# Kernel optimization log

Measured on AMD Instinct MI355X. Metric: run time of the kernel, lower is better.

Reference implementation:

```python
import jax, jax.numpy as jnp
import numpy as np
from jax import lax

T = 16          # timesteps
EPS = 1e-12     # torch F.normalize eps
DN = ('NCHW', 'OIHW', 'NCHW')

def conv2d(x, w, pad):
    return lax.conv_general_dilated(x, w, (1, 1), [(pad, pad), (pad, pad)],
                                    dimension_numbers=DN)

def setup_inputs() -> dict:
    key = jax.random.key(0)
    ks = jax.random.split(key, 7)
    B, C, H, W, K = 16, 512, 14, 14, 64
    return {
        'input_tensor': jax.random.normal(ks[0], (B * T, C, H, W), jnp.float32),
        'centers': jax.random.normal(ks[1], (K, C), jnp.float32) * 0.05,
        'share_w': jax.random.normal(ks[2], (K, C, 1, 1), jnp.float32) * 0.05,
        'share_b': jax.random.uniform(ks[3], (K,), jnp.float32),
        'U_z': jax.random.normal(ks[4], (K, K, 3, 3), jnp.float32) * 0.05,
        'U_r': jax.random.normal(ks[5], (K, K, 3, 3), jnp.float32) * 0.05,
        'U_h': jax.random.normal(ks[6], (K, K, 3, 3), jnp.float32) * 0.05,
    }

def reference(input_tensor, centers, share_w, share_b, U_z, U_r, U_h):
    NT, C, H, W = input_tensor.shape
    B = NT // T
    K = centers.shape[0]

    # soft-assignment pre-activation: 1x1 conv (SAME) -> [B*T, K, H, W]
    wxb = conv2d(input_tensor, share_w, 0) + share_b[None, :, None, None]
    wxb = wxb.reshape(B, T, K, H, W).transpose(1, 0, 2, 3, 4)  # [T,B,K,H,W]

    def gru_step(h, wxb_t):
        z = jax.nn.sigmoid(wxb_t + conv2d(h, U_z, 1))
        r = jax.nn.sigmoid(wxb_t + conv2d(h, U_r, 1))
        hh = jnp.tanh(wxb_t + conv2d(r * h, U_h, 1))
        h_new = (1.0 - z) * hh + z * h
        return h_new, h_new

    h0 = jnp.zeros((B, K, H, W), input_tensor.dtype)
    _, assign = lax.scan(gru_step, h0, wxb)            # [T,B,K,H,W]
    assign = assign.transpose(1, 0, 2, 3, 4).reshape(B * T, K, H * W)

    a_sum = assign.sum(-1, keepdims=True)              # [BT,K,1]
    a = a_sum * centers[None]                          # [BT,K,C]
    feats = input_tensor.reshape(B * T, C, H * W)
    x = jnp.einsum('nks,ncs->nkc', assign, feats)      # [BT,K,C]

    vlad = (x - a).reshape(B, T, K, C).sum(1)          # [B,K,C]
    vlad = vlad / jnp.maximum(jnp.linalg.norm(vlad, axis=2, keepdims=True), EPS)
    vlad = vlad.reshape(B, K * C)
    vlad = vlad / jnp.maximum(jnp.linalg.norm(vlad, axis=1, keepdims=True), EPS)
    return vlad
```

## Files before the change

kernel.cpp:

```cpp
#include <hip/hip_runtime.h>

#define Bc 16
#define Tc 16
#define Cc 512
#define Kc 64
#define Sc 196
#define KS (Kc*Sc)
#define BKS (Bc*Kc*Sc)
#define TBKS (Tc*BKS)
#define GFIN (16*64*512)
#define PART_N (8*GFIN)
#define PX 256
#define PLB2 (Kc*PX)

typedef __attribute__((ext_vector_type(8))) short bf16x8;
typedef __attribute__((ext_vector_type(4))) float f32x4;

__device__ __forceinline__ float sigmoid_f(float x) { return 1.f / (1.f + __expf(-x)); }
__device__ __forceinline__ float tanh_f(float x) { return 1.f - 2.f / (__expf(2.f * x) + 1.f); }

__device__ __forceinline__ float b2f(unsigned short u) {
    return __uint_as_float(((unsigned)u) << 16);
}
__device__ __forceinline__ unsigned short f2b(float f) {
    unsigned u = __float_as_uint(f);
    return (unsigned short)((u + 0x7FFFu + ((u >> 16) & 1u)) >> 16);
}
__device__ __forceinline__ void split1(float f, unsigned short& h, unsigned short& l) {
    unsigned u = __float_as_uint(f);
    unsigned uh = u & 0xffff0000u;
    h = (unsigned short)(uh >> 16);
    float fl = f - __uint_as_float(uh);
    l = (unsigned short)(__float_as_uint(fl) >> 16);
}

__device__ __forceinline__ float dpp_prev(float v) {
    return __int_as_float(__builtin_amdgcn_mov_dpp(__float_as_int(v), 0x111, 0xf, 0xf, true));
}
__device__ __forceinline__ float dpp_next(float v) {
    return __int_as_float(__builtin_amdgcn_mov_dpp(__float_as_int(v), 0x101, 0xf, 0xf, true));
}

__global__ __launch_bounds__(256) void k_prep_w(const float* __restrict__ w,
        unsigned short* __restrict__ wh, unsigned short* __restrict__ wl) {
    int idx = blockIdx.x * 256 + threadIdx.x;
    unsigned short h, l;
    split1(w[idx], h, l);
    wh[idx] = h; wl[idx] = l;
}

__global__ __launch_bounds__(256) void k_init(float4* __restrict__ h32,
        float4* __restrict__ h16, float4* __restrict__ rh16) {
    const int i = blockIdx.x * 256 + threadIdx.x;
    const float4 z = make_float4(0.f, 0.f, 0.f, 0.f);
    h32[i] = z;
    if (i < 32768) { h16[i] = z; rh16[i] = z; }
}

__global__ __launch_bounds__(512) void k_conv1x1(const float* __restrict__ x,
        const unsigned short* __restrict__ wh, const unsigned short* __restrict__ wl,
        const float* __restrict__ bias, float* __restrict__ wxb,
        float* __restrict__ assign0, float* __restrict__ hplane32,
        unsigned short* __restrict__ hplane16) {
    __shared__ unsigned short Xh[64 * 40];
    __shared__ unsigned short Xl[64 * 40];
    const int gs0 = blockIdx.x * 64;
    const int tid = threadIdx.x;
    const int wv = tid >> 6, lane = tid & 63;
    const int lg = lane >> 4, ln = lane & 15;
    const int mt = wv & 3, np = wv >> 2;
    const int gslS = tid & 63;
    const int c4S = (tid >> 6) * 4;
    const int gsS = gs0 + gslS;
    const int nS = gsS / Sc, sS = gsS - nS * Sc;
    const float* xcol = x + (size_t)nS * (Cc * Sc) + sS;
    const int colS = (((c4S >> 3) ^ ((gslS >> 3) & 3)) << 3) + (c4S & 7);
    const int kA = np * 32 + ln;
    const float bias0 = bias[kA], bias1 = bias[kA + 16];
    const int gsA = mt * 16 + ln;
    const int swzA = (gsA >> 3) & 3;

    float xr[4];
#pragma unroll
    for (int i = 0; i < 4; ++i) xr[i] = xcol[(size_t)(c4S + i) * Sc];

    f32x4 acc0 = {0.f, 0.f, 0.f, 0.f}, acc1 = {0.f, 0.f, 0.f, 0.f};
    for (int c0 = 0; c0 < Cc; c0 += 32) {
        __syncthreads();
        {
            ushort4 h, l;
            split1(xr[0], h.x, l.x); split1(xr[1], h.y, l.y);
            split1(xr[2], h.z, l.z); split1(xr[3], h.w, l.w);
            *(ushort4*)(Xh + gslS * 40 + colS) = h;
            *(ushort4*)(Xl + gslS * 40 + colS) = l;
        }
        __syncthreads();
        if (c0 + 32 < Cc) {
#pragma unroll
            for (int i = 0; i < 4; ++i) xr[i] = xcol[(size_t)(c0 + 32 + c4S + i) * Sc];
        }
        bf16x8 B0h = *(const bf16x8*)(wh + (size_t)kA * Cc + c0 + lg * 8);
        bf16x8 B0l = *(const bf16x8*)(wl + (size_t)kA * Cc + c0 + lg * 8);
        bf16x8 B1h = *(const bf16x8*)(wh + (size_t)(kA + 16) * Cc + c0 + lg * 8);
        bf16x8 B1l = *(const bf16x8*)(wl + (size_t)(kA + 16) * Cc + c0 + lg * 8);
        bf16x8 Af = *(const bf16x8*)(Xh + gsA * 40 + ((lg ^ swzA) << 3));
        bf16x8 Alo = *(const bf16x8*)(Xl + gsA * 40 + ((lg ^ swzA) << 3));
        acc0 = __builtin_amdgcn_mfma_f32_16x16x32_bf16(Af, B0h, acc0, 0, 0, 0);
        acc0 = __builtin_amdgcn_mfma_f32_16x16x32_bf16(Alo, B0h, acc0, 0, 0, 0);
        acc0 = __builtin_amdgcn_mfma_f32_16x16x32_bf16(Af, B0l, acc0, 0, 0, 0);
        acc1 = __builtin_amdgcn_mfma_f32_16x16x32_bf16(Af, B1h, acc1, 0, 0, 0);
        acc1 = __builtin_amdgcn_mfma_f32_16x16x32_bf16(Alo, B1h, acc1, 0, 0, 0);
        acc1 = __builtin_amdgcn_mfma_f32_16x16x32_bf16(Af, B1l, acc1, 0, 0, 0);
    }
#pragma unroll
    for (int r = 0; r < 4; ++r) {
        const int gs = gs0 + mt * 16 + lg * 4 + r;
        const int n = gs / Sc, s = gs - (gs / Sc) * Sc;
        const int t = n & 15, bb = n >> 4;
        const float v0 = acc0[r] + bias0;
        const float v1 = acc1[r] + bias1;
        const size_t rowbase = ((size_t)t * Bc + bb) * Kc;
        wxb[(rowbase + kA) * Sc + s] = v0;
        wxb[(rowbase + kA + 16) * Sc + s] = v1;
        if (t == 0) {
            const int px = (s / 14 + 1) * 16 + (s - (s / 14) * 14 + 1);
            const float a0 = (1.f - sigmoid_f(v0)) * tanh_f(v0);
            const float a1 = (1.f - sigmoid_f(v1)) * tanh_f(v1);
            assign0[((size_t)bb * Kc + kA) * Sc + s] = a0;
            assign0[((size_t)bb * Kc + kA + 16) * Sc + s] = a1;
            const size_t pp0 = (size_t)bb * PLB2 + (size_t)kA * PX + px;
            const size_t pp1 = (size_t)bb * PLB2 + (size_t)(kA + 16) * PX + px;
            hplane32[pp0] = a0; hplane16[pp0] = f2b(a0);
            hplane32[pp1] = a1; hplane16[pp1] = f2b(a1);
        }
    }
}

__global__ __launch_bounds__(512) void k_gru_gates(const unsigned short* __restrict__ hplane16,
        const float* __restrict__ wxb_t, const float* __restrict__ Uz, const float* __restrict__ Ur,
        float* __restrict__ zb, unsigned short* __restrict__ rhplane16) {
    extern __shared__ float lds[];
    unsigned short* P = (unsigned short*)lds;
    float* red = lds + 8192;
    const int b = blockIdx.x;
    const int k0 = blockIdx.y * 4;
    const int tid = threadIdx.x;
    const int wv = __builtin_amdgcn_readfirstlane(tid >> 6);
    const int lane = tid & 63;
    const int kp = wv >> 2, kiq = wv & 3;

    float preE[4]; bool valE[4]; size_t csE[4]; int kEa[4];
#pragma unroll
    for (int q = 0; q < 4; ++q) {
        const int o = tid + q * 512;
        const int set = o >> 8, px = o & 255;
        const int kp_o = set >> 2, r = set & 1;
        kEa[q] = k0 + kp_o * 2 + r;
        const int row = px >> 4, col = px & 15;
        valE[q] = (row >= 1 && row <= 14 && col >= 1 && col <= 14);
        csE[q] = ((size_t)b * Kc + kEa[q]) * Sc + (valE[q] ? (row - 1) * 14 + (col - 1) : 0);
        preE[q] = valE[q] ? wxb_t[csE[q]] : 0.f;
    }
    {
        const float4* src = (const float4*)(hplane16 + (size_t)b * PLB2);
        float4* dst = (float4*)P;
#pragma unroll
        for (int it = 0; it < 4; ++it) dst[it * 512 + tid] = src[it * 512 + tid];
    }
    __syncthreads();

    const int yp = lane >> 2, xq = (lane & 3) << 2;
    const int rowbase = (yp > 0) ? (yp - 1) : 0;
    const float* uz0 = Uz + (size_t)(k0 + kp * 2) * 576 + kiq * 144;
    const float* ur0 = Ur + (size_t)(k0 + kp * 2) * 576 + kiq * 144;
    float az[2][4] = {}, ar[2][4] = {};
    const unsigned short* Pw = P + (size_t)(kiq * 16) * PX + rowbase * 16 + xq;
#pragma unroll 2
    for (int ki = 0; ki < 16; ++ki) {
        const unsigned short* pk = Pw + ki * PX;
#pragma unroll
        for (int dy = 0; dy < 3; ++dy) {
            ushort4 u = *(const ushort4*)(pk + dy * 16);
            float4 m = make_float4(b2f(u.x), b2f(u.y), b2f(u.z), b2f(u.w));
            float e0 = dpp_prev(m.w);
            float e4 = dpp_next(m.x);
#pragma unroll
            for (int r = 0; r < 2; ++r) {
                const float* wz = uz0 + r * 576 + ki * 9 + dy * 3;
                float c0 = wz[0], c1 = wz[1], c2 = wz[2];
                az[r][0] += c0*e0  + c1*m.x + c2*m.y;
                az[r][1] += c0*m.x + c1*m.y + c2*m.z;
                az[r][2] += c0*m.y + c1*m.z + c2*m.w;
                az[r][3] += c0*m.z + c1*m.w + c2*e4;
                const float* wr = ur0 + r * 576 + ki * 9 + dy * 3;
                float d0 = wr[0], d1 = wr[1], d2 = wr[2];
                ar[r][0] += d0*e0  + d1*m.x + d2*m.y;
                ar[r][1] += d0*m.x + d1*m.y + d2*m.z;
                ar[r][2] += d0*m.y + d1*m.z + d2*m.w;
                ar[r][3] += d0*m.z + d1*m.w + d2*e4;
            }
        }
    }
    {
        float* rp = red + (size_t)wv * 1024 + lane;
#pragma unroll
        for (int r = 0; r < 2; ++r)
#pragma unroll
            for (int jj = 0; jj < 4; ++jj) {
                rp[(size_t)(r * 4 + jj) * 64] = az[r][jj];
                rp[(size_t)(8 + r * 4 + jj) * 64] = ar[r][jj];
            }
    }
    __syncthreads();
#pragma unroll
    for (int q = 0; q < 4; ++q) {
        const int o = tid + q * 512;
        const int set = o >> 8, px = o & 255;
        const int kp_o = set >> 2, g = (set >> 1) & 1, r = set & 1;
        const int lane_r = ((px >> 4) << 2) + ((px & 15) >> 2);
        const int v = (g * 2 + r) * 4 + (px & 3);
        float s0 = 0.f;
#pragma unroll
        for (int kq2 = 0; kq2 < 4; ++kq2)
            s0 += red[(size_t)((kp_o * 4 + kq2) * 16 + v) * 64 + lane_r];
        if (valE[q]) {
            float sv = sigmoid_f(preE[q] + s0);
            if (g == 0) {
                zb[csE[q]] = sv;
            } else {
                float hv = b2f(P[(size_t)kEa[q] * PX + px]);
                rhplane16[(size_t)b * PLB2 + (size_t)kEa[q] * PX + px] = f2b(sv * hv);
            }
        }
    }
}

__global__ __launch_bounds__(512) void k_gru_out(const unsigned short* __restrict__ rhplane16,
        const float* __restrict__ wxb_t, const float* __restrict__ Uh, const float* __restrict__ zb,
        float* __restrict__ hplane32, unsigned short* __restrict__ hplane16,
        float* __restrict__ assign_t) {
    extern __shared__ float lds[];
    unsigned short* P = (unsigned short*)lds;
    float* red = lds + 8192;
    const int b = blockIdx.x;
    const int k0 = blockIdx.y * 4;
    const int tid = threadIdx.x;
    const int wv = __builtin_amdgcn_readfirstlane(tid >> 6);
    const int lane = tid & 63;
    const int kp = wv >> 2, kiq = wv & 3;

    float preE[2], zvE[2], hpE[2]; bool valE[2]; size_t csE[2], ppE[2];
#pragma unroll
    for (int q = 0; q < 2; ++q) {
        const int o = tid + q * 512;
        const int set = o >> 8, px = o & 255;
        const int kp_o = set >> 1, r = set & 1;
        const int k = k0 + kp_o * 2 + r;
        const int row = px >> 4, col = px & 15;
        valE[q] = (row >= 1 && row <= 14 && col >= 1 && col <= 14);
        csE[q] = ((size_t)b * Kc + k) * Sc + (valE[q] ? (row - 1) * 14 + (col - 1) : 0);
        ppE[q] = (size_t)b * PLB2 + (size_t)k * PX + px;
        preE[q] = 0.f; zvE[q] = 0.f; hpE[q] = 0.f;
        if (valE[q]) {
            preE[q] = wxb_t[csE[q]];
            zvE[q] = zb[csE[q]];
            hpE[q] = hplane32[ppE[q]];
        }
    }
    {
        const float4* src = (const float4*)(rhplane16 + (size_t)b * PLB2);
        float4* dst = (float4*)P;
#pragma unroll
        for (int it = 0; it < 4; ++it) dst[it * 512 + tid] = src[it * 512 + tid];
    }
    __syncthreads();

    const int yp = lane >> 2, xq = (lane & 3) << 2;
    const int rowbase = (yp > 0) ? (yp - 1) : 0;
    const float* uh0 = Uh + (size_t)(k0 + kp * 2) * 576 + kiq * 144;
    float ah[2][4] = {};
    const unsigned short* Pw = P + (size_t)(kiq * 16) * PX + rowbase * 16 + xq;
#pragma unroll 2
    for (int ki = 0; ki < 16; ++ki) {
        const unsigned short* pk = Pw + ki * PX;
#pragma unroll
        for (int dy = 0; dy < 3; ++dy) {
            ushort4 u = *(const ushort4*)(pk + dy * 16);
            float4 m = make_float4(b2f(u.x), b2f(u.y), b2f(u.z), b2f(u.w));
            float e0 = dpp_prev(m.w);
            float e4 = dpp_next(m.x);
#pragma unroll
            for (int r = 0; r < 2; ++r) {
                const float* wh = uh0 + r * 576 + ki * 9 + dy * 3;
                float c0 = wh[0], c1 = wh[1], c2 = wh[2];
                ah[r][0] += c0*e0  + c1*m.x + c2*m.y;
                ah[r][1] += c0*m.x + c1*m.y + c2*m.z;
                ah[r][2] += c0*m.y + c1*m.z + c2*m.w;
                ah[r][3] += c0*m.z + c1*m.w + c2*e4;
            }
        }
    }
    {
        float* rp = red + (size_t)wv * 512 + lane;
#pragma unroll
        for (int r = 0; r < 2; ++r)
#pragma unroll
            for (int jj = 0; jj < 4; ++jj)
                rp[(size_t)(r * 4 + jj) * 64] = ah[r][jj];
    }
    __syncthreads();
#pragma unroll
    for (int q = 0; q < 2; ++q) {
        const int o = tid + q * 512;
        const int set = o >> 8, px = o & 255;
        const int kp_o = set >> 1, r = set & 1;
        const int lane_r = ((px >> 4) << 2) + ((px & 15) >> 2);
        const int v = r * 4 + (px & 3);
        float s0 = 0.f;
#pragma unroll
        for (int kq2 = 0; kq2 < 4; ++kq2)
            s0 += red[(size_t)((kp_o * 4 + kq2) * 8 + v) * 64 + lane_r];
        if (valE[q]) {
            float hh = tanh_f(preE[q] + s0);
            float hn = (1.f - zvE[q]) * hh + zvE[q] * hpE[q];
            hplane32[ppE[q]] = hn;
            hplane16[ppE[q]] = f2b(hn);
            assign_t[csE[q]] = hn;
        }
    }
}

__global__ __launch_bounds__(512) void k_einsum(const float* __restrict__ x, const float* __restrict__ assign,
                                                float* __restrict__ part) {
    extern __shared__ float lds[];
    unsigned short* Ah = (unsigned short*)lds;
    unsigned short* Al = Ah + 64 * 40;
    unsigned short* Xh = Al + 64 * 40;
    unsigned short* Xl = Xh + 128 * 40;
    const int cq = blockIdx.x, tg = blockIdx.y, b = blockIdx.z;
    const int tid = threadIdx.x;
    const int wv = tid >> 6, lane = tid & 63;
    const int lg = lane >> 4, ln = lane & 15;
    const int ka = tid >> 3, ss4 = (tid & 7) * 4;
    const int cx = tid >> 2, ss8 = (tid & 3) * 8;

    f32x4 acc[4];
#pragma unroll
    for (int mt = 0; mt < 4; ++mt) acc[mt] = (f32x4){0.f, 0.f, 0.f, 0.f};

    for (int tt = 0; tt < 2; ++tt) {
        const int t = tg * 2 + tt;
        const int n = b * Tc + t;
        const float* ap = assign + ((size_t)t * Bc + b) * KS;
        const float* xp = x + ((size_t)n * Cc + cq * 128) * Sc;
        for (int sc7 = 0; sc7 < 7; ++sc7) {
            const int s0 = sc7 * 32;
            __syncthreads();
            {
                float4 v = make_float4(0.f, 0.f, 0.f, 0.f);
                if (s0 + ss4 <= 192) v = *(const float4*)(ap + (size_t)ka * Sc + s0 + ss4);
                ushort4 h, l;
                split1(v.x, h.x, l.x); split1(v.y, h.y, l.y);
                split1(v.z, h.z, l.z); split1(v.w, h.w, l.w);
                *(ushort4*)(Ah + ka * 40 + ss4) = h;
                *(ushort4*)(Al + ka * 40 + ss4) = l;
            }
#pragma unroll
            for (int q = 0; q < 2; ++q) {
                const int so = ss8 + q * 4;
                float4 v = make_float4(0.f, 0.f, 0.f, 0.f);
                if (s0 + so <= 192) v = *(const float4*)(xp + (size_t)cx * Sc + s0 + so);
                ushort4 h, l;
                split1(v.x, h.x, l.x); split1(v.y, h.y, l.y);
                split1(v.z, h.z, l.z); split1(v.w, h.w, l.w);
                *(ushort4*)(Xh + cx * 40 + so) = h;
                *(ushort4*)(Xl + cx * 40 + so) = l;
            }
            __syncthreads();
            bf16x8 Bh = *(const bf16x8*)(Xh + (wv * 16 + ln) * 40 + lg * 8);
            bf16x8 Bl = *(const bf16x8*)(Xl + (wv * 16 + ln) * 40 + lg * 8);
#pragma unroll
            for (int mt = 0; mt < 4; ++mt) {
                bf16x8 Af = *(const bf16x8*)(Ah + (mt * 16 + ln) * 40 + lg * 8);
                bf16x8 Alo = *(const bf16x8*)(Al + (mt * 16 + ln) * 40 + lg * 8);
                acc[mt] = __builtin_amdgcn_mfma_f32_16x16x32_bf16(Af, Bh, acc[mt], 0, 0, 0);
                acc[mt] = __builtin_amdgcn_mfma_f32_16x16x32_bf16(Alo, Bh, acc[mt], 0, 0, 0);
                acc[mt] = __builtin_amdgcn_mfma_f32_16x16x32_bf16(Af, Bl, acc[mt], 0, 0, 0);
            }
        }
    }
    const int c = cq * 128 + wv * 16 + ln;
#pragma unroll
    for (int mt = 0; mt < 4; ++mt) {
#pragma unroll
        for (int r = 0; r < 4; ++r) {
            const int k = mt * 16 + lg * 4 + r;
            part[(((size_t)tg * Bc + b) * Kc + k) * Cc + c] = acc[mt][r];
        }
    }
}

__global__ __launch_bounds__(256) void k_reduce(const float* __restrict__ assign, const float* __restrict__ part,
        const float* __restrict__ centers, float* __restrict__ vlad, float* __restrict__ norm2) {
    __shared__ float redw[4];
    __shared__ float a_s;
    const int blk = blockIdx.x;
    const int b = blk >> 6, k = blk & 63;
    const int tid = threadIdx.x;
    const int wave = tid >> 6, lane = tid & 63;
    const size_t bkoff = ((size_t)b * Kc + k) * Sc;
    float s = 0.f;
    for (int q = tid; q < 784; q += 256) {
        int t = q / 49, s4 = q - t * 49;
        float4 v = *(const float4*)(assign + (size_t)t * BKS + bkoff + s4 * 4);
        s += (v.x + v.y) + (v.z + v.w);
    }
#pragma unroll
    for (int o = 1; o < 64; o <<= 1) s += __shfl_xor(s, o);
    if (lane == 0) redw[wave] = s;
    __syncthreads();
    if (tid == 0) a_s = redw[0] + redw[1] + redw[2] + redw[3];
    __syncthreads();
    const float a = a_s;
    const size_t base = ((size_t)b * Kc + k) * Cc;
    const int c = tid * 2;
    float2 acc2 = make_float2(0.f, 0.f);
#pragma unroll
    for (int g = 0; g < 8; ++g) {
        float2 p = *(const float2*)(part + (size_t)g * GFIN + base + c);
        acc2.x += p.x; acc2.y += p.y;
    }
    float2 cv = *(const float2*)(centers + (size_t)k * Cc + c);
    float v0 = acc2.x - a * cv.x, v1 = acc2.y - a * cv.y;
    *(float2*)(vlad + base + c) = make_float2(v0, v1);
    float ss = v0 * v0 + v1 * v1;
#pragma unroll
    for (int o = 1; o < 64; o <<= 1) ss += __shfl_xor(ss, o);
    __syncthreads();
    if (lane == 0) redw[wave] = ss;
    __syncthreads();
    if (tid == 0) norm2[blk] = redw[0] + redw[1] + redw[2] + redw[3];
}

__global__ __launch_bounds__(64) void k_norms(const float* __restrict__ norm2, float* __restrict__ scl) {
    const int b = blockIdx.x;
    const int k = threadIdx.x;
    float ss = norm2[b * Kc + k];
    float inv = 1.f / fmaxf(sqrtf(ss), 1e-12f);
    float g = ss * inv * inv;
#pragma unroll
    for (int o = 1; o < 64; o <<= 1) g += __shfl_xor(g, o);
    float gi = 1.f / fmaxf(sqrtf(g), 1e-12f);
    scl[b * Kc + k] = inv * gi;
}

__global__ __launch_bounds__(256) void k_scale(const float* __restrict__ vlad, const float* __restrict__ scl,
                                               float* __restrict__ out) {
    const int blk = blockIdx.x;
    const int b = blk >> 4, kt = blk & 15;
    const int tid = threadIdx.x;
    const int kk = tid >> 6, lane = tid & 63;
    const int k = kt * 4 + kk;
    const float sv = scl[b * Kc + k];
    const float* vp = vlad + ((size_t)b * Kc + k) * Cc + lane * 8;
    float* op = out + ((size_t)b * Kc + k) * Cc + lane * 8;
    float4 v0 = *(const float4*)vp;
    float4 v1 = *(const float4*)(vp + 4);
    *(float4*)op = make_float4(v0.x * sv, v0.y * sv, v0.z * sv, v0.w * sv);
    *(float4*)(op + 4) = make_float4(v1.x * sv, v1.y * sv, v1.z * sv, v1.w * sv);
}

extern "C" void kernel_launch(void* const* d_in, const int* in_sizes, int n_in,
                              void* d_out, int out_size, void* d_ws, size_t ws_size,
                              hipStream_t stream) {
    (void)in_sizes; (void)n_in; (void)out_size; (void)ws_size;
    const float* x       = (const float*)d_in[0];
    const float* centers = (const float*)d_in[1];
    const float* share_w = (const float*)d_in[2];
    const float* share_b = (const float*)d_in[3];
    const float* Uz      = (const float*)d_in[4];
    const float* Ur      = (const float*)d_in[5];
    const float* Uh      = (const float*)d_in[6];
    float* out = (float*)d_out;
    float* ws  = (float*)d_ws;

    float* part      = ws;
    float* vlad      = ws;
    float* wxb       = ws;
    unsigned short* rhplane16 = (unsigned short*)(ws + (size_t)TBKS);
    unsigned short* hplane16  = (unsigned short*)(ws + (size_t)TBKS + 131072);
    float* assign   = ws + (size_t)PART_N;
    float* zb       = assign + (size_t)TBKS;
    float* hplane32 = zb + (size_t)BKS;
    float* wreg     = hplane32 + (size_t)Bc * PLB2;
    unsigned short* w_hi = (unsigned short*)wreg;
    unsigned short* w_lo = w_hi + (size_t)Kc * Cc;
    float* norm2    = wreg + (size_t)Kc * Cc;
    float* scl      = norm2 + (size_t)Bc * Kc;

    const size_t gates_lds = 65536;
    const size_t outk_lds  = 49152;
    const size_t ein_lds   = (64 * 40 + 128 * 40) * 2 * 2;

    k_prep_w<<<dim3(128), 256, 0, stream>>>(share_w, w_hi, w_lo);
    k_init<<<dim3(256), 256, 0, stream>>>((float4*)hplane32, (float4*)hplane16, (float4*)rhplane16);
    k_conv1x1<<<dim3(784), 512, 0, stream>>>(x, w_hi, w_lo, share_b, wxb,
                                             assign, hplane32, hplane16);
    for (int t = 1; t < Tc; ++t) {
        k_gru_gates<<<dim3(16, 16), 512, gates_lds, stream>>>(hplane16, wxb + (size_t)t * BKS,
                                                              Uz, Ur, zb, rhplane16);
        k_gru_out<<<dim3(16, 16), 512, outk_lds, stream>>>(rhplane16, wxb + (size_t)t * BKS,
                                                           Uh, zb, hplane32, hplane16,
                                                           assign + (size_t)t * BKS);
    }
    k_einsum<<<dim3(4, 8, 16), 512, ein_lds, stream>>>(x, assign, part);
    k_reduce<<<dim3(Bc * Kc), 256, 0, stream>>>(assign, part, centers, vlad, norm2);
    k_norms<<<dim3(Bc), 64, 0, stream>>>(norm2, scl);
    k_scale<<<dim3(256), 256, 0, stream>>>(vlad, scl, out);
}
```

Before: 456.1 us.

## Move GRU 3x3 recurrent convs to bf16 split MFMA with pixel-major hidden layout

The recurrent 3x3 convolutions in the gate and output kernels now run as implicit GEMMs on MFMA bf16 instructions instead of scalar FMAs. The weights are pre-split into hi/lo bf16 parts by a new prep kernel, and the activation is kept as a single bf16 value. The hidden-state planes change from channel-major to pixel-major, so each pixel's 64 channels can be loaded as contiguous MFMA fragments, and the LDS copy uses an XOR swizzle. The cross-wave LDS reduction goes away, but each launch now has only 64 blocks where there were 256, which lowers parallelism on the latency-bound recurrent loop.

```diff
diff --git a/kernel.cpp b/kernel.cpp
--- a/kernel.cpp
+++ b/kernel.cpp
@@ -12,6 +12,7 @@
 #define PART_N (8*GFIN)
 #define PX 256
 #define PLB2 (Kc*PX)
+#define NUTT 110592
 
 typedef __attribute__((ext_vector_type(8))) short bf16x8;
 typedef __attribute__((ext_vector_type(4))) float f32x4;
@@ -34,19 +35,27 @@
     l = (unsigned short)(__float_as_uint(fl) >> 16);
 }
 
-__device__ __forceinline__ float dpp_prev(float v) {
-    return __int_as_float(__builtin_amdgcn_mov_dpp(__float_as_int(v), 0x111, 0xf, 0xf, true));
-}
-__device__ __forceinline__ float dpp_next(float v) {
-    return __int_as_float(__builtin_amdgcn_mov_dpp(__float_as_int(v), 0x101, 0xf, 0xf, true));
-}
-
 __global__ __launch_bounds__(256) void k_prep_w(const float* __restrict__ w,
         unsigned short* __restrict__ wh, unsigned short* __restrict__ wl) {
     int idx = blockIdx.x * 256 + threadIdx.x;
     unsigned short h, l;
     split1(w[idx], h, l);
     wh[idx] = h; wl[idx] = l;
+}
+
+__global__ __launch_bounds__(256) void k_prep_u(const float* __restrict__ Uz,
+        const float* __restrict__ Ur, const float* __restrict__ Uh,
+        unsigned short* __restrict__ uth, unsigned short* __restrict__ utl) {
+    int idx = blockIdx.x * 256 + threadIdx.x;
+    int ki = idx & 63;
+    int ko = (idx >> 6) & 63;
+    int gt = idx >> 12;
+    int tap = gt % 9, g = gt / 9;
+    const float* U = (g == 0) ? Uz : (g == 1) ? Ur : Uh;
+    float v = U[((size_t)ko * 64 + ki) * 9 + tap];
+    unsigned short h, l;
+    split1(v, h, l);
+    uth[idx] = h; utl[idx] = l;
 }
 
 __global__ __launch_bounds__(256) void k_init(float4* __restrict__ h32,
@@ -128,204 +137,184 @@
             const float a1 = (1.f - sigmoid_f(v1)) * tanh_f(v1);
             assign0[((size_t)bb * Kc + kA) * Sc + s] = a0;
             assign0[((size_t)bb * Kc + kA + 16) * Sc + s] = a1;
-            const size_t pp0 = (size_t)bb * PLB2 + (size_t)kA * PX + px;
-            const size_t pp1 = (size_t)bb * PLB2 + (size_t)(kA + 16) * PX + px;
+            const size_t pp0 = (size_t)bb * PLB2 + (size_t)px * 64 + kA;
             hplane32[pp0] = a0; hplane16[pp0] = f2b(a0);
-            hplane32[pp1] = a1; hplane16[pp1] = f2b(a1);
+            hplane32[pp0 + 16] = a1; hplane16[pp0 + 16] = f2b(a1);
         }
     }
 }
 
 __global__ __launch_bounds__(512) void k_gru_gates(const unsigned short* __restrict__ hplane16,
-        const float* __restrict__ wxb_t, const float* __restrict__ Uz, const float* __restrict__ Ur,
+        const float* __restrict__ wxb_t, const unsigned short* __restrict__ uth,
+        const unsigned short* __restrict__ utl,
         float* __restrict__ zb, unsigned short* __restrict__ rhplane16) {
-    extern __shared__ float lds[];
-    unsigned short* P = (unsigned short*)lds;
-    float* red = lds + 8192;
-    const int b = blockIdx.x;
-    const int k0 = blockIdx.y * 4;
+    __shared__ unsigned short P[290 * 64];
+    const int b = blockIdx.x, mh = blockIdx.y, gate = blockIdx.z;
     const int tid = threadIdx.x;
-    const int wv = __builtin_amdgcn_readfirstlane(tid >> 6);
-    const int lane = tid & 63;
-    const int kp = wv >> 2, kiq = wv & 3;
-
-    float preE[4]; bool valE[4]; size_t csE[4]; int kEa[4];
-#pragma unroll
-    for (int q = 0; q < 4; ++q) {
-        const int o = tid + q * 512;
-        const int set = o >> 8, px = o & 255;
-        const int kp_o = set >> 2, r = set & 1;
-        kEa[q] = k0 + kp_o * 2 + r;
-        const int row = px >> 4, col = px & 15;
-        valE[q] = (row >= 1 && row <= 14 && col >= 1 && col <= 14);
-        csE[q] = ((size_t)b * Kc + kEa[q]) * Sc + (valE[q] ? (row - 1) * 14 + (col - 1) : 0);
-        preE[q] = valE[q] ? wxb_t[csE[q]] : 0.f;
+    const int wv = tid >> 6, lane = tid & 63;
+    const int lg = lane >> 4, ln = lane & 15;
+    const int pxb = (mh * 8 + wv) * 16;
+
+    int sE[4]; bool vE[4];
+#pragma unroll
+    for (int r = 0; r < 4; ++r) {
+        int px = pxb + lg * 4 + r;
+        int row = px >> 4, col = px & 15;
+        vE[r] = (row >= 1 && row <= 14 && col >= 1 && col <= 14);
+        sE[r] = vE[r] ? (row - 1) * 14 + col - 1 : 0;
+    }
+    float pre[4][4];
+#pragma unroll
+    for (int nt = 0; nt < 4; ++nt) {
+        const float* wp = wxb_t + ((size_t)b * Kc + nt * 16 + ln) * Sc;
+#pragma unroll
+        for (int r = 0; r < 4; ++r) pre[nt][r] = vE[r] ? wp[sE[r]] : 0.f;
     }
     {
+        const float4 z4 = make_float4(0.f, 0.f, 0.f, 0.f);
+        float4* Pv = (float4*)P;
+        if (tid < 136) { Pv[tid] = z4; Pv[273 * 8 + tid] = z4; }
         const float4* src = (const float4*)(hplane16 + (size_t)b * PLB2);
-        float4* dst = (float4*)P;
-#pragma unroll
-        for (int it = 0; it < 4; ++it) dst[it * 512 + tid] = src[it * 512 + tid];
+#pragma unroll
+        for (int it = 0; it < 4; ++it) {
+            int idx = it * 512 + tid;
+            int px = idx >> 3, c16 = idx & 7;
+            int row = px + 17;
+            int boff = row * 128 + ((c16 * 16) ^ ((row & 7) << 4));
+            *(float4*)((char*)P + boff) = src[idx];
+        }
     }
     __syncthreads();
 
-    const int yp = lane >> 2, xq = (lane & 3) << 2;
-    const int rowbase = (yp > 0) ? (yp - 1) : 0;
-    const float* uz0 = Uz + (size_t)(k0 + kp * 2) * 576 + kiq * 144;
-    const float* ur0 = Ur + (size_t)(k0 + kp * 2) * 576 + kiq * 144;
-    float az[2][4] = {}, ar[2][4] = {};
-    const unsigned short* Pw = P + (size_t)(kiq * 16) * PX + rowbase * 16 + xq;
-#pragma unroll 2
-    for (int ki = 0; ki < 16; ++ki) {
-        const unsigned short* pk = Pw + ki * PX;
-#pragma unroll
-        for (int dy = 0; dy < 3; ++dy) {
-            ushort4 u = *(const ushort4*)(pk + dy * 16);
-            float4 m = make_float4(b2f(u.x), b2f(u.y), b2f(u.z), b2f(u.w));
-            float e0 = dpp_prev(m.w);
-            float e4 = dpp_next(m.x);
-#pragma unroll
-            for (int r = 0; r < 2; ++r) {
-                const float* wz = uz0 + r * 576 + ki * 9 + dy * 3;
-                float c0 = wz[0], c1 = wz[1], c2 = wz[2];
-                az[r][0] += c0*e0  + c1*m.x + c2*m.y;
-                az[r][1] += c0*m.x + c1*m.y + c2*m.z;
-                az[r][2] += c0*m.y + c1*m.z + c2*m.w;
-                az[r][3] += c0*m.z + c1*m.w + c2*e4;
-                const float* wr = ur0 + r * 576 + ki * 9 + dy * 3;
-                float d0 = wr[0], d1 = wr[1], d2 = wr[2];
-                ar[r][0] += d0*e0  + d1*m.x + d2*m.y;
-                ar[r][1] += d0*m.x + d1*m.y + d2*m.z;
-                ar[r][2] += d0*m.y + d1*m.z + d2*m.w;
-                ar[r][3] += d0*m.z + d1*m.w + d2*e4;
+    const unsigned short* uh0 = uth + (size_t)gate * 9 * 4096;
+    const unsigned short* ul0 = utl + (size_t)gate * 9 * 4096;
+    f32x4 acc[4];
+#pragma unroll
+    for (int nt = 0; nt < 4; ++nt) acc[nt] = (f32x4){0.f, 0.f, 0.f, 0.f};
+#pragma unroll
+    for (int tap = 0; tap < 9; ++tap) {
+        const int toff = (tap / 3 - 1) * 16 + (tap % 3 - 1);
+#pragma unroll
+        for (int ks = 0; ks < 2; ++ks) {
+            const int row = pxb + ln + toff + 17;
+            const int boff = row * 128 + ((ks * 64 + lg * 16) ^ ((row & 7) << 4));
+            bf16x8 A = *(const bf16x8*)((const char*)P + boff);
+#pragma unroll
+            for (int nt = 0; nt < 4; ++nt) {
+                const size_t bo = ((size_t)tap * 64 + nt * 16 + ln) * 64 + ks * 32 + lg * 8;
+                bf16x8 Bh = *(const bf16x8*)(uh0 + bo);
+                bf16x8 Bl = *(const bf16x8*)(ul0 + bo);
+                acc[nt] = __builtin_amdgcn_mfma_f32_16x16x32_bf16(A, Bh, acc[nt], 0, 0, 0);
+                acc[nt] = __builtin_amdgcn_mfma_f32_16x16x32_bf16(A, Bl, acc[nt], 0, 0, 0);
             }
         }
     }
-    {
-        float* rp = red + (size_t)wv * 1024 + lane;
-#pragma unroll
-        for (int r = 0; r < 2; ++r)
-#pragma unroll
-            for (int jj = 0; jj < 4; ++jj) {
-                rp[(size_t)(r * 4 + jj) * 64] = az[r][jj];
-                rp[(size_t)(8 + r * 4 + jj) * 64] = ar[r][jj];
+#pragma unroll
+    for (int nt = 0; nt < 4; ++nt) {
+        const int ko = nt * 16 + ln;
+#pragma unroll
+        for (int r = 0; r < 4; ++r) {
+            if (!vE[r]) continue;
+            float sv = sigmoid_f(pre[nt][r] + acc[nt][r]);
+            if (gate == 0) {
+                zb[((size_t)b * Kc + ko) * Sc + sE[r]] = sv;
+            } else {
+                const int px = pxb + lg * 4 + r;
+                const int row = px + 17;
+                const int hoff = row * 128 + ((ko * 2) ^ ((row & 7) << 4));
+                float hv = b2f(*(const unsigned short*)((const char*)P + hoff));
+                rhplane16[(size_t)b * PLB2 + (size_t)px * 64 + ko] = f2b(sv * hv);
             }
-    }
-    __syncthreads();
-#pragma unroll
-    for (int q = 0; q < 4; ++q) {
-        const int o = tid + q * 512;
-        const int set = o >> 8, px = o & 255;
-        const int kp_o = set >> 2, g = (set >> 1) & 1, r = set & 1;
-        const int lane_r = ((px >> 4) << 2) + ((px & 15) >> 2);
-        const int v = (g * 2 + r) * 4 + (px & 3);
-        float s0 = 0.f;
-#pragma unroll
-        for (int kq2 = 0; kq2 < 4; ++kq2)
-            s0 += red[(size_t)((kp_o * 4 + kq2) * 16 + v) * 64 + lane_r];
-        if (valE[q]) {
-            float sv = sigmoid_f(preE[q] + s0);
-            if (g == 0) {
-                zb[csE[q]] = sv;
-            } else {
-                float hv = b2f(P[(size_t)kEa[q] * PX + px]);
-                rhplane16[(size_t)b * PLB2 + (size_t)kEa[q] * PX + px] = f2b(sv * hv);
-            }
         }
     }
 }
 
 __global__ __launch_bounds__(512) void k_gru_out(const unsigned short* __restrict__ rhplane16,
-        const float* __restrict__ wxb_t, const float* __restrict__ Uh, const float* __restrict__ zb,
+        const float* __restrict__ wxb_t, const unsigned short* __restrict__ uth,
+        const unsigned short* __restrict__ utl, const float* __restrict__ zb,
         float* __restrict__ hplane32, unsigned short* __restrict__ hplane16,
         float* __restrict__ assign_t) {
-    extern __shared__ float lds[];
-    unsigned short* P = (unsigned short*)lds;
-    float* red = lds + 8192;
-    const int b = blockIdx.x;
-    const int k0 = blockIdx.y * 4;
+    __shared__ unsigned short P[290 * 64];
+    const int b = blockIdx.x, mh = blockIdx.y, nh = blockIdx.z;
     const int tid = threadIdx.x;
-    const int wv = __builtin_amdgcn_readfirstlane(tid >> 6);
-    const int lane = tid & 63;
-    const int kp = wv >> 2, kiq = wv & 3;
-
-    float preE[2], zvE[2], hpE[2]; bool valE[2]; size_t csE[2], ppE[2];
+    const int wv = tid >> 6, lane = tid & 63;
+    const int lg = lane >> 4, ln = lane & 15;
+    const int pxb = (mh * 8 + wv) * 16;
+
+    int sE[4]; bool vE[4];
+#pragma unroll
+    for (int r = 0; r < 4; ++r) {
+        int px = pxb + lg * 4 + r;
+        int row = px >> 4, col = px & 15;
+        vE[r] = (row >= 1 && row <= 14 && col >= 1 && col <= 14);
+        sE[r] = vE[r] ? (row - 1) * 14 + col - 1 : 0;
+    }
+    float pre[2][4], zv[2][4], hp[2][4];
 #pragma unroll
     for (int q = 0; q < 2; ++q) {
-        const int o = tid + q * 512;
-        const int set = o >> 8, px = o & 255;
-        const int kp_o = set >> 1, r = set & 1;
-        const int k = k0 + kp_o * 2 + r;
-        const int row = px >> 4, col = px & 15;
-        valE[q] = (row >= 1 && row <= 14 && col >= 1 && col <= 14);
-        csE[q] = ((size_t)b * Kc + k) * Sc + (valE[q] ? (row - 1) * 14 + (col - 1) : 0);
-        ppE[q] = (size_t)b * PLB2 + (size_t)k * PX + px;
-        preE[q] = 0.f; zvE[q] = 0.f; hpE[q] = 0.f;
-        if (valE[q]) {
-            preE[q] = wxb_t[csE[q]];
-            zvE[q] = zb[csE[q]];
-            hpE[q] = hplane32[ppE[q]];
+        const int ko = (nh * 2 + q) * 16 + ln;
+        const float* wp = wxb_t + ((size_t)b * Kc + ko) * Sc;
+        const float* zp = zb + ((size_t)b * Kc + ko) * Sc;
+        const float* hpp = hplane32 + (size_t)b * PLB2 + ko;
+#pragma unroll
+        for (int r = 0; r < 4; ++r) {
+            pre[q][r] = vE[r] ? wp[sE[r]] : 0.f;
+            zv[q][r]  = vE[r] ? zp[sE[r]] : 0.f;
+            hp[q][r]  = vE[r] ? hpp[(size_t)(pxb + lg * 4 + r) * 64] : 0.f;
         }
     }
     {
+        const float4 z4 = make_float4(0.f, 0.f, 0.f, 0.f);
+        float4* Pv = (float4*)P;
+        if (tid < 136) { Pv[tid] = z4; Pv[273 * 8 + tid] = z4; }
         const float4* src = (const float4*)(rhplane16 + (size_t)b * PLB2);
-        float4* dst = (float4*)P;
-#pragma unroll
-        for (int it = 0; it < 4; ++it) dst[it * 512 + tid] = src[it * 512 + tid];
+#pragma unroll
+        for (int it = 0; it < 4; ++it) {
+            int idx = it * 512 + tid;
+            int px = idx >> 3, c16 = idx & 7;
+            int row = px + 17;
+            int boff = row * 128 + ((c16 * 16) ^ ((row & 7) << 4));
+            *(float4*)((char*)P + boff) = src[idx];
+        }
     }
     __syncthreads();
 
-    const int yp = lane >> 2, xq = (lane & 3) << 2;
-    const int rowbase = (yp > 0) ? (yp - 1) : 0;
-    const float* uh0 = Uh + (size_t)(k0 + kp * 2) * 576 + kiq * 144;
-    float ah[2][4] = {};
-    const unsigned short* Pw = P + (size_t)(kiq * 16) * PX + rowbase * 16 + xq;
-#pragma unroll 2
-    for (int ki = 0; ki < 16; ++ki) {
-        const unsigned short* pk = Pw + ki * PX;
-#pragma unroll
-        for (int dy = 0; dy < 3; ++dy) {
-            ushort4 u = *(const ushort4*)(pk + dy * 16);
-            float4 m = make_float4(b2f(u.x), b2f(u.y), b2f(u.z), b2f(u.w));
-            float e0 = dpp_prev(m.w);
-            float e4 = dpp_next(m.x);
-#pragma unroll
-            for (int r = 0; r < 2; ++r) {
-                const float* wh = uh0 + r * 576 + ki * 9 + dy * 3;
-                float c0 = wh[0], c1 = wh[1], c2 = wh[2];
-                ah[r][0] += c0*e0  + c1*m.x + c2*m.y;
-                ah[r][1] += c0*m.x + c1*m.y + c2*m.z;
-                ah[r][2] += c0*m.y + c1*m.z + c2*m.w;
-                ah[r][3] += c0*m.z + c1*m.w + c2*e4;
+    const unsigned short* uh0 = uth + (size_t)2 * 9 * 4096;
+    const unsigned short* ul0 = utl + (size_t)2 * 9 * 4096;
+    f32x4 acc[2];
+    acc[0] = (f32x4){0.f, 0.f, 0.f, 0.f};
+    acc[1] = (f32x4){0.f, 0.f, 0.f, 0.f};
+#pragma unroll
+    for (int tap = 0; tap < 9; ++tap) {
+        const int toff = (tap / 3 - 1) * 16 + (tap % 3 - 1);
+#pragma unroll
+        for (int ks = 0; ks < 2; ++ks) {
+            const int row = pxb + ln + toff + 17;
+            const int boff = row * 128 + ((ks * 64 + lg * 16) ^ ((row & 7) << 4));
+            bf16x8 A = *(const bf16x8*)((const char*)P + boff);
+#pragma unroll
+            for (int q = 0; q < 2; ++q) {
+                const size_t bo = ((size_t)tap * 64 + (nh * 2 + q) * 16 + ln) * 64 + ks * 32 + lg * 8;
+                bf16x8 Bh = *(const bf16x8*)(uh0 + bo);
+                bf16x8 Bl = *(const bf16x8*)(ul0 + bo);
+                acc[q] = __builtin_amdgcn_mfma_f32_16x16x32_bf16(A, Bh, acc[q], 0, 0, 0);
+                acc[q] = __builtin_amdgcn_mfma_f32_16x16x32_bf16(A, Bl, acc[q], 0, 0, 0);
             }
         }
     }
-    {
-        float* rp = red + (size_t)wv * 512 + lane;
-#pragma unroll
-        for (int r = 0; r < 2; ++r)
-#pragma unroll
-            for (int jj = 0; jj < 4; ++jj)
-                rp[(size_t)(r * 4 + jj) * 64] = ah[r][jj];
-    }
-    __syncthreads();
 #pragma unroll
     for (int q = 0; q < 2; ++q) {
-        const int o = tid + q * 512;
-        const int set = o >> 8, px = o & 255;
-        const int kp_o = set >> 1, r = set & 1;
-        const int lane_r = ((px >> 4) << 2) + ((px & 15) >> 2);
-        const int v = r * 4 + (px & 3);
-        float s0 = 0.f;
-#pragma unroll
-        for (int kq2 = 0; kq2 < 4; ++kq2)
-            s0 += red[(size_t)((kp_o * 4 + kq2) * 8 + v) * 64 + lane_r];
-        if (valE[q]) {
-            float hh = tanh_f(preE[q] + s0);
-            float hn = (1.f - zvE[q]) * hh + zvE[q] * hpE[q];
-            hplane32[ppE[q]] = hn;
-            hplane16[ppE[q]] = f2b(hn);
-            assign_t[csE[q]] = hn;
+        const int ko = (nh * 2 + q) * 16 + ln;
+#pragma unroll
+        for (int r = 0; r < 4; ++r) {
+            if (!vE[r]) continue;
+            const int px = pxb + lg * 4 + r;
+            float hh = tanh_f(pre[q][r] + acc[q][r]);
+            float hn = (1.f - zv[q][r]) * hh + zv[q][r] * hp[q][r];
+            const size_t pp = (size_t)b * PLB2 + (size_t)px * 64 + ko;
+            hplane32[pp] = hn;
+            hplane16[pp] = f2b(hn);
+            assign_t[((size_t)b * Kc + ko) * Sc + sE[r]] = hn;
         }
     }
 }
@@ -495,23 +484,25 @@
     float* wreg     = hplane32 + (size_t)Bc * PLB2;
     unsigned short* w_hi = (unsigned short*)wreg;
     unsigned short* w_lo = w_hi + (size_t)Kc * Cc;
-    float* norm2    = wreg + (size_t)Kc * Cc;
+    unsigned short* utt_h = (unsigned short*)(wreg + (size_t)Kc * Cc / 2 * 2 / 2 + 16384);
+    utt_h = (unsigned short*)(wreg + 32768);
+    unsigned short* utt_l = utt_h + NUTT;
+    float* norm2    = wreg + 32768 + NUTT;
     float* scl      = norm2 + (size_t)Bc * Kc;
 
-    const size_t gates_lds = 65536;
-    const size_t outk_lds  = 49152;
-    const size_t ein_lds   = (64 * 40 + 128 * 40) * 2 * 2;
+    const size_t ein_lds = (64 * 40 + 128 * 40) * 2 * 2;
 
     k_prep_w<<<dim3(128), 256, 0, stream>>>(share_w, w_hi, w_lo);
+    k_prep_u<<<dim3(432), 256, 0, stream>>>(Uz, Ur, Uh, utt_h, utt_l);
     k_init<<<dim3(256), 256, 0, stream>>>((float4*)hplane32, (float4*)hplane16, (float4*)rhplane16);
     k_conv1x1<<<dim3(784), 512, 0, stream>>>(x, w_hi, w_lo, share_b, wxb,
                                              assign, hplane32, hplane16);
     for (int t = 1; t < Tc; ++t) {
-        k_gru_gates<<<dim3(16, 16), 512, gates_lds, stream>>>(hplane16, wxb + (size_t)t * BKS,
-                                                              Uz, Ur, zb, rhplane16);
-        k_gru_out<<<dim3(16, 16), 512, outk_lds, stream>>>(rhplane16, wxb + (size_t)t * BKS,
-                                                           Uh, zb, hplane32, hplane16,
-                                                           assign + (size_t)t * BKS);
+        k_gru_gates<<<dim3(16, 2, 2), 512, 0, stream>>>(hplane16, wxb + (size_t)t * BKS,
+                                                        utt_h, utt_l, zb, rhplane16);
+        k_gru_out<<<dim3(16, 2, 2), 512, 0, stream>>>(rhplane16, wxb + (size_t)t * BKS,
+                                                      utt_h, utt_l, zb, hplane32, hplane16,
+                                                      assign + (size_t)t * BKS);
     }
     k_einsum<<<dim3(4, 8, 16), 512, ein_lds, stream>>>(x, assign, part);
     k_reduce<<<dim3(Bc * Kc), 256, 0, stream>>>(assign, part, centers, vlad, norm2);
```

Result: slower. 992.0 us (+117.5%).
